# Kernel tuning notes

Measured on AMD Instinct MI355X. Metric: run time of the kernel, lower is better.

Reference implementation:

```python
import jax, jax.numpy as jnp
import numpy as np

KERNEL_SIZE = 5   # from __init__ default
SIGMA_S = 1.0     # spatial gaussian sigma (both axes)
SIGMA_R = 0.04    # range (color) gaussian sigma


def _space_kernel(k, sigma):
    # kornia-style 1D gaussian, normalized to sum 1, then outer product -> (k, k)
    x = jnp.arange(k, dtype=jnp.float32) - (k // 2)
    g = jnp.exp(-(x * x) / (2.0 * sigma * sigma))
    g = g / g.sum()
    return jnp.outer(g, g)


def setup_inputs() -> dict:
    key = jax.random.key(0)
    images = jax.random.uniform(key, (16, 512, 512, 3), dtype=jnp.float32)  # [B,H,W,3] in [0,1]
    return {"images": images}


def reference(images):
    k = KERNEL_SIZE
    pad = k // 2
    x = jnp.transpose(images, (0, 3, 1, 2))  # (B, C, H, W)
    B, C, H, W = x.shape
    xp = jnp.pad(x, ((0, 0), (0, 0), (pad, pad), (pad, pad)), mode="reflect")
    sk = _space_kernel(k, SIGMA_S).astype(x.dtype)
    inv2sr2 = 0.5 / (SIGMA_R * SIGMA_R)
    num = jnp.zeros_like(x)
    den = jnp.zeros((B, 1, H, W), dtype=x.dtype)
    # fused accumulation over the k*k window (fixed 25-tap loop, fully vectorized per tap)
    for dy in range(k):
        for dx in range(k):
            sh = xp[:, :, dy:dy + H, dx:dx + W]                  # shifted neighbor (B,C,H,W)
            d2 = jnp.sum((sh - x) ** 2, axis=1, keepdims=True)   # color distance^2 (B,1,H,W)
            w = sk[dy, dx] * jnp.exp(-inv2sr2 * d2)              # space * range weight
            num = num + w * sh
            den = den + w
    out = jnp.clip(num / den, 0.0, 1.0)
    return jnp.transpose(out, (0, 2, 3, 1))  # back to (B, H, W, C)
```

## Files before the change

kernel.cpp:

```cpp
#include <hip/hip_runtime.h>
#include <math.h>

#define IMG_H 512
#define IMG_W 512
#define CH    3
#define TILE  16
#define PAD   2
#define TP    (TILE + 2 * PAD)

typedef float v2f __attribute__((ext_vector_type(2)));

#if __has_builtin(__builtin_amdgcn_exp2f)
#define EXP2(x) __builtin_amdgcn_exp2f(x)
#else
#define EXP2(x) exp2f(x)
#endif

#if __has_builtin(__builtin_amdgcn_rcpf)
#define RCP(x) __builtin_amdgcn_rcpf(x)
#else
#define RCP(x) (1.0f / (x))
#endif

__device__ __forceinline__ int reflect_idx(int i, int n) {
    i = (i < 0) ? -i : i;
    i = (i >= n) ? (2 * n - 2 - i) : i;
    return i;
}

__global__ __launch_bounds__(256)
void bilateral_kernel(const float* __restrict__ in, float* __restrict__ out) {
    __shared__ float4 lds[TP][TP];

    const float S = sqrtf(312.5f * 1.44269504088896f);

    const int b  = blockIdx.z;
    const int by = blockIdx.y * TILE;
    const int bx = blockIdx.x * TILE;
    const int tx = threadIdx.x;
    const int ty = threadIdx.y;
    const int tid = ty * TILE + tx;

    for (int i = tid; i < TP * TP; i += 256) {
        const int py = i / TP;
        const int px = i - py * TP;
        const int gy = reflect_idx(by + py - PAD, IMG_H);
        const int gx = reflect_idx(bx + px - PAD, IMG_W);
        const float* src = in + ((size_t)(b * IMG_H + gy) * IMG_W + gx) * CH;
        const float s0 = src[0] * S;
        const float s1 = src[1] * S;
        const float s2 = src[2] * S;
        const float mq = -fmaf(s0, s0, fmaf(s1, s1, s2 * s2));
        ((float4*)lds)[i] = make_float4(s0, s1, s2, mq);
    }
    __syncthreads();

    const int rp = ((ty & 3) << 2) | (ty >> 2);

    const float CW[3] = { -4.1978935f, -2.0338538f, -1.3125121f };

    const float4 c = lds[rp + PAD][tx + PAD];
    const v2f c01  = (v2f){ c.x + c.x, c.y + c.y };
    const v2f c2z1 = (v2f){ c.z + c.z, 1.0f };
    const float cw0 = c.w + CW[0];
    const float cw1 = c.w + CW[1];
    const float cw2 = c.w + CW[2];
    const float cwd[5] = { cw0, cw1, cw2, cw1, cw0 };

    v2f   nxy = (v2f){ 0.0f, 0.0f };
    float n2 = 0.0f, den = 0.0f;

    #pragma unroll
    for (int dy = 0; dy < 5; ++dy) {
        const v2f base0 = (v2f){ cwd[dy], 0.0f };
        #pragma unroll
        for (int k = 0; k < 5; ++k) {
            float4 s = lds[rp + dy][tx + k];
            s.w += CW[k < 3 ? k : 4 - k];
            const v2f sxy = (v2f){ s.x, s.y };
            const v2f szw = (v2f){ s.z, s.w };
            const v2f q = __builtin_elementwise_fma(szw, c2z1, base0);
            const v2f p = __builtin_elementwise_fma(sxy, c01, q);
            const float w = EXP2(p.x + p.y);
            nxy = __builtin_elementwise_fma((v2f){ w, w }, sxy, nxy);
            n2  = fmaf(w, s.z, n2);
            den += w;
        }
    }

    const float inv = RCP(den * S);
    const int y = by + rp;
    const int x = bx + tx;
    float* dst = out + ((size_t)(b * IMG_H + y) * IMG_W + x) * CH;
    dst[0] = fminf(fmaxf(nxy.x * inv, 0.0f), 1.0f);
    dst[1] = fminf(fmaxf(nxy.y * inv, 0.0f), 1.0f);
    dst[2] = fminf(fmaxf(n2   * inv, 0.0f), 1.0f);
}

extern "C" void kernel_launch(void* const* d_in, const int* in_sizes, int n_in,
                              void* d_out, int out_size, void* d_ws, size_t ws_size,
                              hipStream_t stream) {
    const float* in = (const float*)d_in[0];
    float* out = (float*)d_out;
    const int B = in_sizes[0] / (IMG_H * IMG_W * CH);

    dim3 block(TILE, TILE, 1);
    dim3 grid(IMG_W / TILE, IMG_H / TILE, B);
    bilateral_kernel<<<grid, block, 0, stream>>>(in, out);
}
```

Baseline: 42.52 us.

## Compute two output rows per thread with interleaved packed-math planes

Each thread now produces two pixels, sixteen rows apart, using a 16x32 tile. Shared memory holds two interleaved planes, so every packed v2f operation works on both pixels at once and all FMAs map onto packed instructions. The aim is to use packed FP32 math fully and to halve the number of blocks launched. The cost is higher register pressure and two 16-byte shared-memory loads per tap, and the two halos are loaded separately, so no halo rows are shared between the two halves.

```diff
diff --git a/kernel.cpp b/kernel.cpp
--- a/kernel.cpp
+++ b/kernel.cpp
@@ -4,11 +4,14 @@
 #define IMG_H 512
 #define IMG_W 512
 #define CH    3
-#define TILE  16
+#define TILE_W 16
+#define TILE_H 32
+#define HALF  16
 #define PAD   2
-#define TP    (TILE + 2 * PAD)
+#define TP    20
 
 typedef float v2f __attribute__((ext_vector_type(2)));
+typedef float v4f __attribute__((ext_vector_type(4)));
 
 #if __has_builtin(__builtin_amdgcn_exp2f)
 #define EXP2(x) __builtin_amdgcn_exp2f(x)
@@ -30,28 +33,32 @@
 
 __global__ __launch_bounds__(256)
 void bilateral_kernel(const float* __restrict__ in, float* __restrict__ out) {
-    __shared__ float4 lds[TP][TP];
+    __shared__ v4f planeP[TP][TP];
+    __shared__ v4f planeQ[TP][TP];
 
     const float S = sqrtf(312.5f * 1.44269504088896f);
 
     const int b  = blockIdx.z;
-    const int by = blockIdx.y * TILE;
-    const int bx = blockIdx.x * TILE;
+    const int by = blockIdx.y * TILE_H;
+    const int bx = blockIdx.x * TILE_W;
     const int tx = threadIdx.x;
     const int ty = threadIdx.y;
-    const int tid = ty * TILE + tx;
+    const int tid = ty * TILE_W + tx;
 
     for (int i = tid; i < TP * TP; i += 256) {
-        const int py = i / TP;
-        const int px = i - py * TP;
-        const int gy = reflect_idx(by + py - PAD, IMG_H);
-        const int gx = reflect_idx(bx + px - PAD, IMG_W);
-        const float* src = in + ((size_t)(b * IMG_H + gy) * IMG_W + gx) * CH;
-        const float s0 = src[0] * S;
-        const float s1 = src[1] * S;
-        const float s2 = src[2] * S;
-        const float mq = -fmaf(s0, s0, fmaf(s1, s1, s2 * s2));
-        ((float4*)lds)[i] = make_float4(s0, s1, s2, mq);
+        const int r  = i / TP;
+        const int cc = i - r * TP;
+        const int gyA = reflect_idx(by + r - PAD, IMG_H);
+        const int gyB = reflect_idx(by + HALF + r - PAD, IMG_H);
+        const int gx  = reflect_idx(bx + cc - PAD, IMG_W);
+        const float* pA = in + ((size_t)(b * IMG_H + gyA) * IMG_W + gx) * CH;
+        const float* pB = in + ((size_t)(b * IMG_H + gyB) * IMG_W + gx) * CH;
+        const float a0 = pA[0] * S, a1 = pA[1] * S, a2 = pA[2] * S;
+        const float e0 = pB[0] * S, e1 = pB[1] * S, e2 = pB[2] * S;
+        const float wA = -fmaf(a0, a0, fmaf(a1, a1, a2 * a2));
+        const float wB = -fmaf(e0, e0, fmaf(e1, e1, e2 * e2));
+        planeP[r][cc] = (v4f){ a0, e0, a1, e1 };
+        planeQ[r][cc] = (v4f){ a2, e2, wA, wB };
     }
     __syncthreads();
 
@@ -59,42 +66,64 @@
 
     const float CW[3] = { -4.1978935f, -2.0338538f, -1.3125121f };
 
-    const float4 c = lds[rp + PAD][tx + PAD];
-    const v2f c01  = (v2f){ c.x + c.x, c.y + c.y };
-    const v2f c2z1 = (v2f){ c.z + c.z, 1.0f };
-    const float cw0 = c.w + CW[0];
-    const float cw1 = c.w + CW[1];
-    const float cw2 = c.w + CW[2];
-    const float cwd[5] = { cw0, cw1, cw2, cw1, cw0 };
+    const v4f cP = planeP[rp + PAD][tx + PAD];
+    const v4f cQ = planeQ[rp + PAD][tx + PAD];
+    const v2f c2x = __builtin_shufflevector(cP, cP, 0, 1) + __builtin_shufflevector(cP, cP, 0, 1);
+    const v2f c2y = __builtin_shufflevector(cP, cP, 2, 3) + __builtin_shufflevector(cP, cP, 2, 3);
+    const v2f c2z = __builtin_shufflevector(cQ, cQ, 0, 1) + __builtin_shufflevector(cQ, cQ, 0, 1);
+    const v2f cw  = __builtin_shufflevector(cQ, cQ, 2, 3);
 
-    v2f   nxy = (v2f){ 0.0f, 0.0f };
-    float n2 = 0.0f, den = 0.0f;
+    v2f base[3][3];
+    #pragma unroll
+    for (int iy = 0; iy < 3; ++iy)
+        #pragma unroll
+        for (int ix = 0; ix < 3; ++ix) {
+            const float k = CW[iy] + CW[ix];
+            base[iy][ix] = cw + (v2f){ k, k };
+        }
+
+    v2f nx = (v2f){0.f,0.f}, ny = (v2f){0.f,0.f};
+    v2f nz = (v2f){0.f,0.f}, nd = (v2f){0.f,0.f};
 
     #pragma unroll
     for (int dy = 0; dy < 5; ++dy) {
-        const v2f base0 = (v2f){ cwd[dy], 0.0f };
+        const int iy = (dy < 3) ? dy : 4 - dy;
         #pragma unroll
         for (int k = 0; k < 5; ++k) {
-            float4 s = lds[rp + dy][tx + k];
-            s.w += CW[k < 3 ? k : 4 - k];
-            const v2f sxy = (v2f){ s.x, s.y };
-            const v2f szw = (v2f){ s.z, s.w };
-            const v2f q = __builtin_elementwise_fma(szw, c2z1, base0);
-            const v2f p = __builtin_elementwise_fma(sxy, c01, q);
-            const float w = EXP2(p.x + p.y);
-            nxy = __builtin_elementwise_fma((v2f){ w, w }, sxy, nxy);
-            n2  = fmaf(w, s.z, n2);
-            den += w;
+            const int ix = (k < 3) ? k : 4 - k;
+            const v4f P = planeP[rp + dy][tx + k];
+            const v4f Q = planeQ[rp + dy][tx + k];
+            const v2f sx = __builtin_shufflevector(P, P, 0, 1);
+            const v2f sy = __builtin_shufflevector(P, P, 2, 3);
+            const v2f sz = __builtin_shufflevector(Q, Q, 0, 1);
+            const v2f sw = __builtin_shufflevector(Q, Q, 2, 3);
+            v2f t = sw + base[iy][ix];
+            t = __builtin_elementwise_fma(sz, c2z, t);
+            t = __builtin_elementwise_fma(sy, c2y, t);
+            t = __builtin_elementwise_fma(sx, c2x, t);
+            const v2f w = (v2f){ EXP2(t.x), EXP2(t.y) };
+            nx = __builtin_elementwise_fma(w, sx, nx);
+            ny = __builtin_elementwise_fma(w, sy, ny);
+            nz = __builtin_elementwise_fma(w, sz, nz);
+            nd = nd + w;
         }
     }
 
-    const float inv = RCP(den * S);
-    const int y = by + rp;
-    const int x = bx + tx;
-    float* dst = out + ((size_t)(b * IMG_H + y) * IMG_W + x) * CH;
-    dst[0] = fminf(fmaxf(nxy.x * inv, 0.0f), 1.0f);
-    dst[1] = fminf(fmaxf(nxy.y * inv, 0.0f), 1.0f);
-    dst[2] = fminf(fmaxf(n2   * inv, 0.0f), 1.0f);
+    const int xcol = bx + tx;
+    {
+        const float inv = RCP(nd.x * S);
+        float* dst = out + ((size_t)(b * IMG_H + by + rp) * IMG_W + xcol) * CH;
+        dst[0] = fminf(fmaxf(nx.x * inv, 0.0f), 1.0f);
+        dst[1] = fminf(fmaxf(ny.x * inv, 0.0f), 1.0f);
+        dst[2] = fminf(fmaxf(nz.x * inv, 0.0f), 1.0f);
+    }
+    {
+        const float inv = RCP(nd.y * S);
+        float* dst = out + ((size_t)(b * IMG_H + by + HALF + rp) * IMG_W + xcol) * CH;
+        dst[0] = fminf(fmaxf(nx.y * inv, 0.0f), 1.0f);
+        dst[1] = fminf(fmaxf(ny.y * inv, 0.0f), 1.0f);
+        dst[2] = fminf(fmaxf(nz.y * inv, 0.0f), 1.0f);
+    }
 }
 
 extern "C" void kernel_launch(void* const* d_in, const int* in_sizes, int n_in,
@@ -104,7 +133,7 @@
     float* out = (float*)d_out;
     const int B = in_sizes[0] / (IMG_H * IMG_W * CH);
 
-    dim3 block(TILE, TILE, 1);
-    dim3 grid(IMG_W / TILE, IMG_H / TILE, B);
+    dim3 block(TILE_W, 16, 1);
+    dim3 grid(IMG_W / TILE_W, IMG_H / TILE_H, B);
     bilateral_kernel<<<grid, block, 0, stream>>>(in, out);
 }
```

After: 38.24 us. 10.1% less time.
